# Performance work log

Hardware: AMD Instinct MI355X
Metric: run time of the kernel (lower is better)

The kernel has to match this reference:

```python
import jax, jax.numpy as jnp
import numpy as np

B, T, D, H, DK, DV, FF = 4, 1024, 1024, 16, 64, 64, 4096


def setup_inputs() -> dict:
    key = jax.random.key(0)
    ks = jax.random.split(key, 16)
    sc = 0.02  # init scale (original uses uninitialized torch.empty; use small randn)
    n = lambda k, shape: jax.random.normal(k, shape, jnp.float32) * sc
    return dict(
        x=jax.random.normal(ks[0], (B, T, D), jnp.float32),
        y=jax.random.normal(ks[1], (B, T, D), jnp.float32),
        Wq1=n(ks[2], (H, D, DK)), Wk1=n(ks[3], (H, D, DK)),
        Wv1=n(ks[4], (H, D, DV)), Wo1=n(ks[5], (D, D)),
        Wq2=n(ks[6], (H, D, DK)), Wk2=n(ks[7], (H, D, DK)),
        Wv2=n(ks[8], (H, D, DV)), Wo2=n(ks[9], (D, D)),
        W_in=n(ks[10], (FF, D)), b_in=jnp.zeros((FF,), jnp.float32),
        W_out=n(ks[11], (D, FF)), b_out=jnp.zeros((D,), jnp.float32),
    )


def _mha(q, k, v, Wq, Wk, Wv, Wo):
    # per-head projections: (B,T,D) x (H,D,dk) -> (B,H,T,dk)
    WQ = jnp.einsum('btd,hdk->bhtk', q, Wq)
    WK = jnp.einsum('bsd,hdk->bhsk', k, Wk)
    WV = jnp.einsum('bsd,hdv->bhsv', v, Wv)
    scores = jnp.einsum('bhtk,bhsk->bhts', WQ, WK) / jnp.sqrt(jnp.float32(DK))
    # NOTE: original code softmaxes over dim=2 (the QUERY axis), kept faithfully
    attn = jax.nn.softmax(scores, axis=2)
    partial = jnp.einsum('bhts,bhsv->bhtv', attn, WV)
    partial = partial.transpose(0, 2, 1, 3).reshape(q.shape[0], q.shape[1], -1)  # (B,T,H*dv)
    return partial @ Wo


def _sub_norm(o):
    mean = o.mean(-1, keepdims=True)
    std = o.std(-1, ddof=1, keepdims=True)  # torch.std default is unbiased
    return o - mean - std  # faithful: subtract (not divide by) std


def reference(x, y, Wq1, Wk1, Wv1, Wo1, Wq2, Wk2, Wv2, Wo2, W_in, b_in, W_out, b_out):
    out1 = _sub_norm(_mha(y, y, y, Wq1, Wk1, Wv1, Wo1) + y)
    out2 = _sub_norm(_mha(y, x, x, Wq2, Wk2, Wv2, Wo2) + out1)
    ff = jax.nn.relu(y @ W_in.T + b_in) @ W_out.T + b_out  # FFN applied to y, as in source
    return _sub_norm(ff + out2)
```

## Files before the change

kernel.cpp:

```cpp
#include <hip/hip_runtime.h>


typedef unsigned short u16;
typedef __bf16 bf16x8 __attribute__((ext_vector_type(8)));
typedef float f32x4 __attribute__((ext_vector_type(4)));

__device__ __forceinline__ u16 f2bf(float f) {
    unsigned int u = __float_as_uint(f);
    u += 0x7fffu + ((u >> 16) & 1u);
    return (u16)(u >> 16);
}
__device__ __forceinline__ float bf2f(u16 b) {
    return __uint_as_float(((unsigned int)b) << 16);
}

typedef __attribute__((address_space(1))) const void* as1cv;
typedef __attribute__((address_space(3))) void* as3v;
__device__ __forceinline__ void gl_lds16(const void* g, void* l) {
    __builtin_amdgcn_global_load_lds((as1cv)g, (as3v)l, 16, 0, 0);
}

__global__ __launch_bounds__(256) void mega_pack_k(
    const float* __restrict__ yf, u16* __restrict__ yb,
    const float* __restrict__ xf, u16* __restrict__ xb,
    const float* __restrict__ W_in, u16* __restrict__ Winb,
    const float* __restrict__ W_out, u16* __restrict__ Woutb,
    const float* __restrict__ Wq1, const float* __restrict__ Wk1,
    const float* __restrict__ Wv1, const float* __restrict__ Wq2,
    u16* __restrict__ W1cat,
    const float* __restrict__ Wk2, const float* __restrict__ Wv2,
    u16* __restrict__ Wkv2t,
    const float* __restrict__ Wo1, u16* __restrict__ Wo1t,
    const float* __restrict__ Wo2, u16* __restrict__ Wo2t)
{
    __shared__ float tile[64][65];
    int id = blockIdx.x;
    if (id < 16384) {
        int j = id >> 12, local = id & 4095;
        const float* in; u16* out;
        switch (j) {
            case 0:  in = yf;    out = yb;    break;
            case 1:  in = xf;    out = xb;    break;
            case 2:  in = W_in;  out = Winb;  break;
            default: in = W_out; out = Woutb; break;
        }
        long i = (long)local * 256 + threadIdx.x;
        float4 v = reinterpret_cast<const float4*>(in)[i];
        ushort4 o;
        o.x = f2bf(v.x); o.y = f2bf(v.y); o.z = f2bf(v.z); o.w = f2bf(v.w);
        reinterpret_cast<ushort4*>(out)[i] = o;
        return;
    }
    int t = id - 16384;
    int pj = t >> 8, local = t & 255;
    const float* in; u16* out;
    int Q, R, bx, by, bz;
    if (pj < 6) {
        switch (pj) {
            case 0:  in = Wq1; out = W1cat;           break;
            case 1:  in = Wk1; out = W1cat + 1048576; break;
            case 2:  in = Wv1; out = W1cat + 2097152; break;
            case 3:  in = Wq2; out = W1cat + 3145728; break;
            case 4:  in = Wk2; out = Wkv2t;           break;
            default: in = Wv2; out = Wkv2t + 1048576; break;
        }
        Q = 1024; R = 64; bx = 0; by = local & 15; bz = local >> 4;
    } else {
        in = (pj == 6) ? Wo1 : Wo2; out = (pj == 6) ? Wo1t : Wo2t;
        Q = 1024; R = 1024; bx = local & 15; by = local >> 4; bz = 0;
    }
    int r0 = bx * 64, q0 = by * 64;
    int tx = threadIdx.x & 63, ty = threadIdx.x >> 6;
    const float* inp = in + ((long)bz * Q + q0) * R + r0;
    #pragma unroll
    for (int i = 0; i < 64; i += 4)
        tile[ty + i][tx] = inp[(long)(ty + i) * R + tx];
    __syncthreads();
    u16* outp = out + ((long)bz * R + r0) * Q + q0;
    #pragma unroll
    for (int i = 0; i < 64; i += 4)
        outp[(long)(ty + i) * Q + tx] = f2bf(tile[tx][ty + i]);
}

__global__ __launch_bounds__(256) void transpose_scale_k(
    const u16* __restrict__ in, long ld_in, long z_in,
    u16* __restrict__ out, long ld_out, long z_out,
    const float* __restrict__ csum) {
    __shared__ u16 tile[64][66];
    int z = blockIdx.z;
    const u16* inz = in + (long)z * z_in;
    u16* outz = out + (long)z * z_out;
    int r0 = blockIdx.y * 64;
    int c0 = blockIdx.x * 64;
    int tx = threadIdx.x & 63, ty = threadIdx.x >> 6;
    #pragma unroll
    for (int i = 0; i < 64; i += 4)
        tile[ty + i][tx] = inz[(long)(r0 + ty + i) * ld_in + c0 + tx];
    __syncthreads();
    #pragma unroll
    for (int i = 0; i < 64; i += 4) {
        int orow = c0 + ty + i;
        float f = bf2f(tile[tx][ty + i]) / csum[(long)z * 16384 + (orow >> 6) * 1024 + r0 + tx];
        outz[(long)orow * ld_out + r0 + tx] = f2bf(f);
    }
}

template<int BM, int BN, int BK, int WM, int WN, int OUT_BF16, int EPI, int SWZ, int KS>
__global__ __launch_bounds__(256) void gemm_k(
    const u16* __restrict__ A, long lda, long a_zin, long a_zout,
    const u16* __restrict__ B, long ldb, long b_zin, long b_zout,
    void* __restrict__ Cv, long ldc, long c_zin, long c_zout,
    int zin, int K, float alpha, const float* __restrict__ bias,
    float* __restrict__ csum)
{
    static_assert(BK == 64, "staging assumes BK=64");
    constexpr int WTM = BM / WM;
    constexpr int WTN = BN / WN;
    constexpr int TM = WTM / 16;
    constexpr int TN = WTN / 16;
    __shared__ __align__(16) u16 smem[(BM + BN) * BK];
    u16* As = smem;
    u16* Bs = smem + BM * BK;

    int bx, by, z;
    if (SWZ == 4) {
        int L = blockIdx.x;
        if (KS > 1) { z = L >> 9; L &= 511; } else { z = 0; }
        by = (L & 7) * 4 + ((L >> 3) & 3);
        bx = L >> 5;
    } else {
        bx = blockIdx.x; by = blockIdx.y; z = blockIdx.z;
    }
    int zi = z % zin, zo = z / zin;
    A += (long)zi * a_zin + (long)zo * a_zout;
    B += (long)zi * b_zin + (long)zo * b_zout;
    long coff = (long)zi * c_zin + (long)zo * c_zout;

    int tid = threadIdx.x;
    int lane = tid & 63;
    int wave = tid >> 6;
    int wm = wave / WN, wn = wave % WN;
    long bm0 = (long)by * BM, bn0 = (long)bx * BN;

    f32x4 acc[TM][TN];
    #pragma unroll
    for (int i = 0; i < TM; ++i)
        #pragma unroll
        for (int j = 0; j < TN; ++j) {
            acc[i][j][0] = 0.f; acc[i][j][1] = 0.f;
            acc[i][j][2] = 0.f; acc[i][j][3] = 0.f;
        }

    int r16 = lane & 15;
    int quad = lane >> 4;
    int l8 = lane >> 3;
    int gsw = ((lane & 7) ^ l8) * 8;

    constexpr int ASTR = BM / 8;
    constexpr int BSTR = BN / 8;

    for (int k0 = 0; k0 < K; k0 += BK) {
        #pragma unroll
        for (int s = wave; s < ASTR; s += 4)
            gl_lds16(&A[(bm0 + s * 8 + l8) * lda + k0 + gsw], &As[s * 512]);
        #pragma unroll
        for (int s = wave; s < BSTR; s += 4)
            gl_lds16(&B[(bn0 + s * 8 + l8) * ldb + k0 + gsw], &Bs[s * 512]);
        __syncthreads();
        #pragma unroll
        for (int kk = 0; kk < BK; kk += 32) {
            int cb = (kk >> 3) + quad;
            bf16x8 av[TM], bv[TN];
            #pragma unroll
            for (int i = 0; i < TM; ++i) {
                int r = wm * WTM + i * 16 + r16;
                av[i] = *reinterpret_cast<const bf16x8*>(&As[r * 64 + ((cb ^ (r & 7)) * 8)]);
            }
            #pragma unroll
            for (int j = 0; j < TN; ++j) {
                int r = wn * WTN + j * 16 + r16;
                bv[j] = *reinterpret_cast<const bf16x8*>(&Bs[r * 64 + ((cb ^ (r & 7)) * 8)]);
            }
            #pragma unroll
            for (int i = 0; i < TM; ++i)
                #pragma unroll
                for (int j = 0; j < TN; ++j)
                    acc[i][j] = __builtin_amdgcn_mfma_f32_16x16x32_bf16(av[i], bv[j], acc[i][j], 0, 0, 0);
        }
        __syncthreads();
    }

    int rb = quad * 4;

    if (EPI == 4) {
        float csl[TN];
        #pragma unroll
        for (int j = 0; j < TN; ++j) csl[j] = 0.f;
        #pragma unroll
        for (int i = 0; i < TM; ++i)
            #pragma unroll
            for (int j = 0; j < TN; ++j)
                #pragma unroll
                for (int r = 0; r < 4; ++r)
                    csl[j] += __expf(acc[i][j][r] * alpha);
        #pragma unroll
        for (int j = 0; j < TN; ++j) {
            float cs = csl[j];
            cs += __shfl_xor(cs, 16, 64);
            cs += __shfl_xor(cs, 32, 64);
            if (quad == 0) {
                long col = bn0 + wn * WTN + j * 16 + r16;
                atomicAdd(&csum[((long)zo * zin + zi) * 1024 + col], cs);
            }
        }
        return;
    }

    constexpr int EB = OUT_BF16 ? 2 : 4;
    constexpr int CH = 16 / EB;
    constexpr int STRIDE = BN + CH;
    constexpr int LDSB = (BM + BN) * BK * 2;
    constexpr int EPASS = (BM * STRIDE * EB > LDSB) ? 2 : 1;
    constexpr int RPP = BM / EPASS;
    static_assert(RPP * STRIDE * EB <= LDSB, "epilogue tile overflows LDS");
    static_assert(EPASS == 1 || (WM == 2 && WTM == RPP), "pass/wave row alignment");
    constexpr int CPR = BN / CH;
    constexpr int NCH = RPP * CPR / 256;
    static_assert(RPP * CPR % 256 == 0, "store mapping");

    float* Ef = reinterpret_cast<float*>(smem);
    char* Cb = reinterpret_cast<char*>(Cv);

    for (int pass = 0; pass < EPASS; ++pass) {
        int p0 = pass * RPP;
        __syncthreads();
        #pragma unroll
        for (int i = 0; i < TM; ++i) {
            #pragma unroll
            for (int j = 0; j < TN; ++j) {
                int lcol = wn * WTN + j * 16 + r16;
                float bsv = (EPI == 1 || EPI == 2) ? bias[bn0 + lcol] : 0.f;
                #pragma unroll
                for (int r = 0; r < 4; ++r) {
                    int lrow = wm * WTM + i * 16 + rb + r;
                    if ((unsigned)(lrow - p0) < (unsigned)RPP) {
                        float v = acc[i][j][r] * alpha;
                        if (EPI == 1) { v += bsv; v = v > 0.f ? v : 0.f; }
                        else if (EPI == 2) { v += bsv; }
                        if (OUT_BF16) smem[(lrow - p0) * STRIDE + lcol] = f2bf(v);
                        else          Ef[(lrow - p0) * STRIDE + lcol] = v;
                    }
                }
            }
        }
        __syncthreads();
        #pragma unroll
        for (int c = 0; c < NCH; ++c) {
            int cid = tid + c * 256;
            int row = cid / CPR, ch = cid - row * CPR;
            int4 v = *reinterpret_cast<const int4*>(
                reinterpret_cast<const char*>(smem) + (row * STRIDE + ch * CH) * EB);
            long gidx = coff + (bm0 + p0 + row) * ldc + bn0 + ch * CH;
            *reinterpret_cast<int4*>(Cb + gidx * EB) = v;
        }
    }
}


__device__ __forceinline__ void bar_raw() {
    asm volatile("" ::: "memory");
    __builtin_amdgcn_s_barrier();
    asm volatile("" ::: "memory");
}

template<int N> __device__ __forceinline__ void vmw() {
    if constexpr (N == 10) asm volatile("s_waitcnt vmcnt(10)" ::: "memory");
    else if constexpr (N == 8) asm volatile("s_waitcnt vmcnt(8)" ::: "memory");
    else if constexpr (N == 4) asm volatile("s_waitcnt vmcnt(4)" ::: "memory");
    else if constexpr (N == 2) asm volatile("s_waitcnt vmcnt(2)" ::: "memory");
    else if constexpr (N == 0) asm volatile("s_waitcnt vmcnt(0)" ::: "memory");
}

__device__ __forceinline__ void stage_half(const u16* __restrict__ base, long ld, int kt,
                                           u16* __restrict__ lds, int half, int wave) {
    const u16* src = base + (long)kt * 64;
    #pragma unroll
    for (int u = 0; u < 2; ++u) {
        int s = half * 16 + u * 8 + wave;
        gl_lds16(src + (long)(s * 8) * ld, lds + s * 512);
    }
}

template<int IH>
__device__ __forceinline__ void read_a8(bf16x8 (&av)[4][2], const u16* __restrict__ As,
                                        int wm, int r16, int quad) {
    #pragma unroll
    for (int ii = 0; ii < 4; ++ii) {
        int r = IH * 128 + wm * 64 + ii * 16 + r16;
        #pragma unroll
        for (int kx = 0; kx < 2; ++kx)
            av[ii][kx] = *reinterpret_cast<const bf16x8*>(&As[r * 64 + (((kx * 4 + quad) ^ (r & 7)) * 8)]);
    }
}

template<int JH>
__device__ __forceinline__ void read_b8(bf16x8 (&bv)[2][2], const u16* __restrict__ Bs,
                                        int wn, int r16, int quad) {
    #pragma unroll
    for (int j = 0; j < 2; ++j) {
        int r = JH * 128 + wn * 32 + j * 16 + r16;
        #pragma unroll
        for (int kx = 0; kx < 2; ++kx)
            bv[j][kx] = *reinterpret_cast<const bf16x8*>(&Bs[r * 64 + (((kx * 4 + quad) ^ (r & 7)) * 8)]);
    }
}

template<int IH, int JH>
__device__ __forceinline__ void mfma_q(f32x4 (&acc)[2][4][2][2],
                                       const bf16x8 (&av)[4][2], const bf16x8 (&bv)[2][2]) {
    #pragma unroll
    for (int kx = 0; kx < 2; ++kx)
        #pragma unroll
        for (int ii = 0; ii < 4; ++ii)
            #pragma unroll
            for (int j = 0; j < 2; ++j)
                acc[IH][ii][JH][j] = __builtin_amdgcn_mfma_f32_16x16x32_bf16(
                    av[ii][kx], bv[j][kx], acc[IH][ii][JH][j], 0, 0, 0);
}

template<int MODE>
__device__ __forceinline__ void tile_iter(
    int t, f32x4 (&acc)[2][4][2][2], bf16x8 (&av)[4][2], bf16x8 (&bvh)[2][2][2],
    u16* __restrict__ smem, const u16* __restrict__ Ab, long lda,
    const u16* __restrict__ Bb, long ldb, int wave, int wm, int wn, int r16, int quad)
{
    u16* As0 = smem + (t & 1) * 32768;
    u16* Bs0 = As0 + 16384;
    u16* As1 = smem + ((t + 1) & 1) * 32768;
    read_a8<0>(av, As0, wm, r16, quad);
    read_b8<0>(bvh[0], Bs0, wn, r16, quad);
    if (MODE < 2) stage_half(Ab, lda, t + 1, As1, 1, wave);
    vmw<MODE == 0 ? 10 : (MODE == 1 ? 10 : 2)>();
    bar_raw(); __builtin_amdgcn_sched_barrier(0);
    __builtin_amdgcn_s_setprio(1);
    mfma_q<0, 0>(acc, av, bvh[0]);
    __builtin_amdgcn_s_setprio(0);
    __builtin_amdgcn_sched_barrier(0);
    bar_raw();
    read_b8<1>(bvh[1], Bs0, wn, r16, quad);
    if (MODE == 0) stage_half(Ab, lda, t + 2, As0, 0, wave);
    vmw<MODE == 0 ? 10 : (MODE == 1 ? 8 : 0)>();
    bar_raw(); __builtin_amdgcn_sched_barrier(0);
    __builtin_amdgcn_s_setprio(1);
    mfma_q<0, 1>(acc, av, bvh[1]);
    __builtin_amdgcn_s_setprio(0);
    __builtin_amdgcn_sched_barrier(0);
    bar_raw();
    read_a8<1>(av, As0, wm, r16, quad);
    if (MODE == 0) stage_half(Bb, ldb, t + 2, Bs0, 0, wave);
    bar_raw(); __builtin_amdgcn_sched_barrier(0);
    __builtin_amdgcn_s_setprio(1);
    mfma_q<1, 0>(acc, av, bvh[0]);
    __builtin_amdgcn_s_setprio(0);
    __builtin_amdgcn_sched_barrier(0);
    bar_raw();
    if (MODE == 0) stage_half(Bb, ldb, t + 2, Bs0, 1, wave);
    if (MODE < 2) vmw<MODE == 0 ? 10 : 4>();
    bar_raw(); __builtin_amdgcn_sched_barrier(0);
    __builtin_amdgcn_s_setprio(1);
    mfma_q<1, 1>(acc, av, bvh[1]);
    __builtin_amdgcn_s_setprio(0);
    __builtin_amdgcn_sched_barrier(0);
    bar_raw();
}

template<int NT, int KS, int EPI, int OUT_BF16, int SPLITN>
__global__ __launch_bounds__(512, 2) void gemm8_k(
    const u16* __restrict__ A, long lda,
    const u16* __restrict__ B, long ldb,
    void* __restrict__ Cv, void* __restrict__ Cv2, long ldc,
    int K, float alpha, const float* __restrict__ bias, long czs)
{
    __shared__ __align__(16) u16 smem[65536];

    int L = blockIdx.x;
    int z = 0;
    if (KS > 1) { z = L / (16 * NT); L -= z * 16 * NT; }
    int by = (L & 7) * 2 + ((L >> 3) & 1);
    int bx = L >> 4;
    if (KS > 1) { A += (long)z * K; B += (long)z * K; }

    int tid = threadIdx.x;
    int lane = tid & 63, wave = tid >> 6;
    int wm = wave >> 2, wn = wave & 3;
    int r16 = lane & 15, quad = lane >> 4, l8 = lane >> 3;
    int gsw = ((lane & 7) ^ l8) * 8;
    long bm0 = (long)by * 256, bn0 = (long)bx * 256;
    const u16* Ab = A + (bm0 + l8) * lda + gsw;
    const u16* Bb = B + (bn0 + l8) * ldb + gsw;

    f32x4 acc[2][4][2][2];
    #pragma unroll
    for (int a0 = 0; a0 < 2; ++a0)
        #pragma unroll
        for (int a1 = 0; a1 < 4; ++a1)
            #pragma unroll
            for (int a2 = 0; a2 < 2; ++a2)
                #pragma unroll
                for (int a3 = 0; a3 < 2; ++a3) {
                    acc[a0][a1][a2][a3][0] = 0.f; acc[a0][a1][a2][a3][1] = 0.f;
                    acc[a0][a1][a2][a3][2] = 0.f; acc[a0][a1][a2][a3][3] = 0.f;
                }
    bf16x8 av[4][2];
    bf16x8 bvh[2][2][2];

    int T = K >> 6;

    stage_half(Ab, lda, 0, smem,         0, wave);
    stage_half(Bb, ldb, 0, smem + 16384, 0, wave);
    stage_half(Bb, ldb, 0, smem + 16384, 1, wave);
    stage_half(Ab, lda, 0, smem,         1, wave);
    stage_half(Ab, lda, 1, smem + 32768, 0, wave);
    stage_half(Bb, ldb, 1, smem + 49152, 0, wave);
    stage_half(Bb, ldb, 1, smem + 49152, 1, wave);
    vmw<10>();
    bar_raw();

    for (int t = 0; t < T - 2; ++t)
        tile_iter<0>(t, acc, av, bvh, smem, Ab, lda, Bb, ldb, wave, wm, wn, r16, quad);
    tile_iter<1>(T - 2, acc, av, bvh, smem, Ab, lda, Bb, ldb, wave, wm, wn, r16, quad);
    tile_iter<2>(T - 1, acc, av, bvh, smem, Ab, lda, Bb, ldb, wave, wm, wn, r16, quad);

    constexpr int EB = OUT_BF16 ? 2 : 4;
    constexpr int EPASS = OUT_BF16 ? 1 : 2;
    bool sec = SPLITN && (bx >= NT / 2);
    char* Cb;
    long bnc = bn0;
    if (SPLITN) {
        Cb = reinterpret_cast<char*>(sec ? Cv2 : Cv);
        if (sec) bnc = bn0 - (long)(NT / 2) * 256;
    } else {
        Cb = reinterpret_cast<char*>((KS > 1 && z >= 2) ? Cv2 : Cv);
        if (KS > 1) Cb += (long)(z & 1) * czs * EB;
    }
    bool do_bias = (EPI == 1) || sec;
    float bsv[2][2];
    if (do_bias) {
        #pragma unroll
        for (int jh = 0; jh < 2; ++jh)
            #pragma unroll
            for (int j = 0; j < 2; ++j)
                bsv[jh][j] = bias[bnc + jh * 128 + wn * 32 + j * 16 + r16];
    }
    u16* sm16 = smem;
    float* smf = reinterpret_cast<float*>(smem);
    #pragma unroll
    for (int pass = 0; pass < EPASS; ++pass) {
        bar_raw();
        #pragma unroll
        for (int ih = 0; ih < 2; ++ih) {
            if (EPASS == 2 && ih != pass) continue;
            #pragma unroll
            for (int ii = 0; ii < 4; ++ii)
                #pragma unroll
                for (int jh = 0; jh < 2; ++jh)
                    #pragma unroll
                    for (int j = 0; j < 2; ++j)
                        #pragma unroll
                        for (int r = 0; r < 4; ++r) {
                            int lrow = (EPASS == 2 ? 0 : ih * 128) + wm * 64 + ii * 16 + quad * 4 + r;
                            int lcol = jh * 128 + wn * 32 + j * 16 + r16;
                            float v = acc[ih][ii][jh][j][r] * alpha;
                            if (do_bias) { v += bsv[jh][j]; v = v > 0.f ? v : 0.f; }
                            int scol = lcol ^ ((lrow & 7) * 8);
                            if (OUT_BF16) sm16[lrow * 256 + scol] = f2bf(v);
                            else          smf[lrow * 256 + scol] = v;
                        }
        }
        bar_raw();
        constexpr int CH = 16 / EB;
        constexpr int CPR = 256 / CH;
        constexpr int NCH = (OUT_BF16 ? 256 : 128) * CPR / 512;
        #pragma unroll
        for (int c = 0; c < NCH; ++c) {
            int cid = tid + c * 512;
            int row = cid / CPR, ch = cid - row * CPR;
            int col = (ch * CH) ^ ((row & 7) * 8);
            int4 v = *reinterpret_cast<const int4*>(
                reinterpret_cast<const char*>(smem) + ((long)row * 256 + col) * EB);
            long grow = bm0 + pass * 128 + row;
            *reinterpret_cast<int4*>(Cb + (grow * ldc + bnc + ch * CH) * EB) = v;
        }
    }
}

__global__ __launch_bounds__(256) void attn_pv_k(
    const u16* __restrict__ Qg, long ldq, long qbz,
    const u16* __restrict__ Kg, long ldk, long kbz,
    const u16* __restrict__ Vg,
    u16* __restrict__ outg)
{
    __shared__ __align__(16) u16 Qs[128 * 64];
    __shared__ __align__(16) u16 Ks[2][64 * 64];
    __shared__ __align__(16) u16 Vs[2][64 * 64];
    __shared__ __align__(16) u16 Es[128 * 64];

    int L = blockIdx.x;
    int h  = (L & 7) * 2 + ((L >> 3) & 1);
    int tb = (L >> 4) & 7;
    int b  = L >> 7;

    const u16* Q  = Qg + (long)b * qbz + h * 64;
    const u16* Kp = Kg + (long)b * kbz + h * 64;
    const u16* Vp = Vg + (long)b * 1048576 + (long)h * 65536;
    u16* outp = outg + (long)b * 1048576 + (long)tb * 131072 + h * 64;

    int tid = threadIdx.x, lane = tid & 63, wave = tid >> 6;
    int wm = wave >> 1, wn = wave & 1;
    int r16 = lane & 15, quad = lane >> 4, l8 = lane >> 3;
    int gsw = ((lane & 7) ^ l8) * 8;
    long t0 = (long)tb * 128;

    #pragma unroll
    for (int s = wave; s < 16; s += 4)
        gl_lds16(&Q[(t0 + s * 8 + l8) * ldq + gsw], &Qs[s * 512]);
    #pragma unroll
    for (int s = wave; s < 8; s += 4) {
        gl_lds16(&Kp[(long)(s * 8 + l8) * ldk + gsw], &Ks[0][s * 512]);
        gl_lds16(&Vp[(long)(s * 8 + l8) * 1024 + gsw], &Vs[0][s * 512]);
    }

    f32x4 acc[4][2];
    #pragma unroll
    for (int i = 0; i < 4; ++i)
        #pragma unroll
        for (int j = 0; j < 2; ++j) {
            acc[i][j][0] = 0.f; acc[i][j][1] = 0.f;
            acc[i][j][2] = 0.f; acc[i][j][3] = 0.f;
        }

    for (int sc = 0; sc < 16; ++sc) {
        const u16* Ksc = Ks[sc & 1];
        const u16* Vsc = Vs[sc & 1];
        if (sc < 15) {
            int nc = sc + 1;
            u16* Kn = Ks[nc & 1];
            u16* Vn = Vs[nc & 1];
            #pragma unroll
            for (int s = wave; s < 8; s += 4) {
                gl_lds16(&Kp[(long)(nc * 64 + s * 8 + l8) * ldk + gsw], &Kn[s * 512]);
                gl_lds16(&Vp[(long)(s * 8 + l8) * 1024 + nc * 64 + gsw], &Vn[s * 512]);
            }
            asm volatile("s_waitcnt vmcnt(4)" ::: "memory");
        } else {
            asm volatile("s_waitcnt vmcnt(0)" ::: "memory");
        }
        bar_raw();

        f32x4 e[4][2];
        #pragma unroll
        for (int i = 0; i < 4; ++i)
            #pragma unroll
            for (int j = 0; j < 2; ++j) {
                e[i][j][0] = 0.f; e[i][j][1] = 0.f;
                e[i][j][2] = 0.f; e[i][j][3] = 0.f;
            }
        #pragma unroll
        for (int kk = 0; kk < 64; kk += 32) {
            int cb = (kk >> 3) + quad;
            bf16x8 av[4], bv[2];
            #pragma unroll
            for (int i = 0; i < 4; ++i) {
                int r = wm * 64 + i * 16 + r16;
                av[i] = *reinterpret_cast<const bf16x8*>(&Qs[r * 64 + ((cb ^ (r & 7)) * 8)]);
            }
            #pragma unroll
            for (int j = 0; j < 2; ++j) {
                int r = wn * 32 + j * 16 + r16;
                bv[j] = *reinterpret_cast<const bf16x8*>(&Ksc[r * 64 + ((cb ^ (r & 7)) * 8)]);
            }
            #pragma unroll
            for (int i = 0; i < 4; ++i)
                #pragma unroll
                for (int j = 0; j < 2; ++j)
                    e[i][j] = __builtin_amdgcn_mfma_f32_16x16x32_bf16(av[i], bv[j], e[i][j], 0, 0, 0);
        }
        #pragma unroll
        for (int i = 0; i < 4; ++i)
            #pragma unroll
            for (int j = 0; j < 2; ++j) {
                int lcol = wn * 32 + j * 16 + r16;
                #pragma unroll
                for (int r = 0; r < 4; ++r) {
                    int lrow = wm * 64 + i * 16 + quad * 4 + r;
                    float v = __expf(e[i][j][r] * 0.125f);
                    Es[lrow * 64 + (((lcol >> 3) ^ (lrow & 7)) * 8) + (lcol & 7)] = f2bf(v);
                }
            }
        asm volatile("s_waitcnt lgkmcnt(0)" ::: "memory");
        bar_raw();

        #pragma unroll
        for (int kk = 0; kk < 64; kk += 32) {
            int cb = (kk >> 3) + quad;
            bf16x8 av[4], bv[2];
            #pragma unroll
            for (int i = 0; i < 4; ++i) {
                int r = wm * 64 + i * 16 + r16;
                av[i] = *reinterpret_cast<const bf16x8*>(&Es[r * 64 + ((cb ^ (r & 7)) * 8)]);
            }
            #pragma unroll
            for (int j = 0; j < 2; ++j) {
                int r = wn * 32 + j * 16 + r16;
                bv[j] = *reinterpret_cast<const bf16x8*>(&Vsc[r * 64 + ((cb ^ (r & 7)) * 8)]);
            }
            #pragma unroll
            for (int i = 0; i < 4; ++i)
                #pragma unroll
                for (int j = 0; j < 2; ++j)
                    acc[i][j] = __builtin_amdgcn_mfma_f32_16x16x32_bf16(av[i], bv[j], acc[i][j], 0, 0, 0);
        }
        bar_raw();
    }

    #pragma unroll
    for (int i = 0; i < 4; ++i)
        #pragma unroll
        for (int j = 0; j < 2; ++j) {
            int lcol = wn * 32 + j * 16 + r16;
            #pragma unroll
            for (int r = 0; r < 4; ++r) {
                int lrow = wm * 64 + i * 16 + quad * 4 + r;
                outp[(long)lrow * 1024 + lcol] = f2bf(acc[i][j][r]);
            }
        }
}

template<int NP, int BIAS>
__global__ __launch_bounds__(256) void addsn_k(const float* __restrict__ parts,
                                               const float* __restrict__ parts2,
                                               long pstride,
                                               const float* __restrict__ resid,
                                               const float* __restrict__ bias,
                                               float* __restrict__ out) {
    __shared__ float sm[8];
    long row = blockIdx.x;
    int tid = threadIdx.x;
    float4 x = reinterpret_cast<const float4*>(resid + row * 1024)[tid];
    #pragma unroll
    for (int p = 0; p < NP; ++p) {
        const float* src = (p < 2) ? (parts + p * pstride) : (parts2 + (p - 2) * pstride);
        float4 a = reinterpret_cast<const float4*>(src + row * 1024)[tid];
        x.x += a.x; x.y += a.y; x.z += a.z; x.w += a.w;
    }
    if (BIAS) {
        float4 bb = reinterpret_cast<const float4*>(bias)[tid];
        x.x += bb.x; x.y += bb.y; x.z += bb.z; x.w += bb.w;
    }
    float s = x.x + x.y + x.z + x.w;
    for (int o = 32; o > 0; o >>= 1) s += __shfl_down(s, o, 64);
    int lane = tid & 63, w = tid >> 6;
    if (lane == 0) sm[w] = s;
    __syncthreads();
    float mean = (sm[0] + sm[1] + sm[2] + sm[3]) * (1.f / 1024.f);
    float d0 = x.x - mean, d1 = x.y - mean, d2 = x.z - mean, d3 = x.w - mean;
    float q = d0 * d0 + d1 * d1 + d2 * d2 + d3 * d3;
    for (int o = 32; o > 0; o >>= 1) q += __shfl_down(q, o, 64);
    if (lane == 0) sm[w + 4] = q;
    __syncthreads();
    float sd = sqrtf((sm[4] + sm[5] + sm[6] + sm[7]) * (1.f / 1023.f));
    float4 ov;
    ov.x = d0 - sd; ov.y = d1 - sd; ov.z = d2 - sd; ov.w = d3 - sd;
    reinterpret_cast<float4*>(out + row * 1024)[tid] = ov;
}


extern "C" void kernel_launch(void* const* d_in, const int* in_sizes, int n_in,
                              void* d_out, int out_size, void* d_ws, size_t ws_size,
                              hipStream_t stream) {
    (void)in_sizes; (void)n_in; (void)out_size; (void)ws_size;
    const float* xf   = (const float*)d_in[0];
    const float* yf   = (const float*)d_in[1];
    const float* Wq1  = (const float*)d_in[2];
    const float* Wk1  = (const float*)d_in[3];
    const float* Wv1  = (const float*)d_in[4];
    const float* Wo1  = (const float*)d_in[5];
    const float* Wq2  = (const float*)d_in[6];
    const float* Wk2  = (const float*)d_in[7];
    const float* Wv2  = (const float*)d_in[8];
    const float* Wo2  = (const float*)d_in[9];
    const float* W_in = (const float*)d_in[10];
    const float* b_in = (const float*)d_in[11];
    const float* W_out= (const float*)d_in[12];
    const float* b_out= (const float*)d_in[13];

    char* p = (char*)d_ws;
    auto alloc = [&](size_t bytes) { char* r = p; p += bytes; return r; };
    u16*   yb    = (u16*)alloc(8388608);
    u16*   xb    = (u16*)alloc(8388608);
    u16*   W1cat = (u16*)alloc(8388608);
    u16*   Winb  = (u16*)alloc(8388608);
    u16*   Wkv2t = (u16*)alloc(4194304);
    u16*   Wo1t  = (u16*)alloc(2097152);
    u16*   Wo2t  = (u16*)alloc(2097152);
    u16*   Woutb = (u16*)alloc(8388608);
    u16*   QKV   = (u16*)alloc(33554432);
    u16*   KV2   = (u16*)alloc(16777216);
    u16*   Vt    = (u16*)alloc(8388608);
    u16*   Pb    = (u16*)alloc(33554432);
    float* csum  = (float*)alloc(262144);
    u16*   part  = (u16*)alloc(8388608);
    float* gout  = (float*)alloc(33554432);
    float* out1  = (float*)alloc(16777216);

    mega_pack_k<<<18432, 256, 0, stream>>>(
        yf, yb, xf, xb, W_in, Winb, W_out, Woutb,
        Wq1, Wk1, Wv1, Wq2, W1cat, Wk2, Wv2, Wkv2t,
        Wo1, Wo1t, Wo2, Wo2t);

    auto run_attention = [&](const u16* Q, long ldq, long qbz,
                             const u16* Kp, long ldk, long kbz,
                             const u16* Vp, long ldv, long vbz) {
        hipMemsetAsync(csum, 0, 262144, stream);
        gemm_k<128,128,64,2,2,1,4,0,1><<<dim3(8, 8, 64), 256, 0, stream>>>(
            Q, ldq, 64L, qbz, Kp, ldk, 64L, kbz,
            (void*)Pb, 1024L, 0L, 0L, 16, 64, 0.125f, nullptr, csum);
        transpose_scale_k<<<dim3(16, 16, 4), 256, 0, stream>>>(
            Vp, ldv, vbz, Vt, 1024L, 1048576L, csum);
        attn_pv_k<<<512, 256, 0, stream>>>(Q, ldq, qbz, Kp, ldk, kbz, Vt, part);
    };

    gemm8_k<32,1,0,1,1><<<512, 512, 0, stream>>>(
        yb, 1024L, W1cat, 1024L, (void*)QKV, (void*)Pb, 4096L, 1024, 1.0f, b_in, 0L);
    gemm8_k<8,1,0,1,0><<<128, 512, 0, stream>>>(
        xb, 1024L, Wkv2t, 1024L, (void*)KV2, nullptr, 2048L, 1024, 1.0f, nullptr, 0L);

    run_attention(QKV, 4096L, 4194304L, QKV + 1024, 4096L, 4194304L, QKV + 2048, 4096L, 4194304L);
    gemm_k<128,64,64,2,2,0,0,4,2><<<dim3(2 * 512), 256, 0, stream>>>(
        part, 1024L, 0L, 512L, Wo1t, 1024L, 0L, 512L,
        (void*)gout, 1024L, 0L, 4194304L, 1, 512, 1.0f, nullptr, nullptr);
    addsn_k<2,0><<<4096, 256, 0, stream>>>(gout, nullptr, 4194304L, yf, nullptr, out1);

    run_attention(QKV + 3072, 4096L, 4194304L, KV2, 2048L, 2097152L, KV2 + 1024, 2048L, 2097152L);
    gemm_k<128,64,64,2,2,0,0,4,2><<<dim3(2 * 512), 256, 0, stream>>>(
        part, 1024L, 0L, 512L, Wo2t, 1024L, 0L, 512L,
        (void*)gout, 1024L, 0L, 4194304L, 1, 512, 1.0f, nullptr, nullptr);
    addsn_k<2,0><<<4096, 256, 0, stream>>>(gout, nullptr, 4194304L, out1, nullptr, (float*)d_out);

    gemm8_k<4,4,0,0,0><<<256, 512, 0, stream>>>(
        Pb, 4096L, Woutb, 4096L, (void*)gout, (void*)QKV, 1024L, 1024, 1.0f, nullptr, 4194304L);
    addsn_k<4,1><<<4096, 256, 0, stream>>>(gout, (const float*)QKV, 4194304L,
                                           (const float*)d_out, b_out, (float*)d_out);
}
```

Before: 508.0 us.

## Batch both attention blocks into merged launches and fold memset into pack kernel

Runs the two attention passes (self and cross) together: one QK gemm launch over 128 z-slices, one merged V transpose/scale, and one PV kernel over 1024 blocks. The two output-projection gemms now run as a single split-style gemm, and the csum zeroing moves into extra blocks of the pack kernel instead of a memset. Workspace buffers are aliased to fit the doubled intermediates. This cuts launch count and fills the GPU better with larger grids, at the cost of more memory and careful buffer reuse.

```diff
diff --git a/kernel.cpp b/kernel.cpp
--- a/kernel.cpp
+++ b/kernel.cpp
@@ -31,10 +31,17 @@
     const float* __restrict__ Wk2, const float* __restrict__ Wv2,
     u16* __restrict__ Wkv2t,
     const float* __restrict__ Wo1, u16* __restrict__ Wo1t,
-    const float* __restrict__ Wo2, u16* __restrict__ Wo2t)
+    const float* __restrict__ Wo2, u16* __restrict__ Wo2t,
+    float* __restrict__ csumz)
 {
     __shared__ float tile[64][65];
     int id = blockIdx.x;
+    if (id >= 18432) {
+        long i = (long)(id - 18432) * 256 + threadIdx.x;
+        float4 zz; zz.x = 0.f; zz.y = 0.f; zz.z = 0.f; zz.w = 0.f;
+        reinterpret_cast<float4*>(csumz)[i] = zz;
+        return;
+    }
     if (id < 16384) {
         int j = id >> 12, local = id & 4095;
         const float* in; u16* out;
@@ -82,36 +89,43 @@
         outp[(long)(ty + i) * Q + tx] = f2bf(tile[tx][ty + i]);
 }
 
-__global__ __launch_bounds__(256) void transpose_scale_k(
-    const u16* __restrict__ in, long ld_in, long z_in,
-    u16* __restrict__ out, long ld_out, long z_out,
-    const float* __restrict__ csum) {
+__global__ __launch_bounds__(256) void tscale2_k(
+    const u16* __restrict__ in1, long ld1, long zs1,
+    const u16* __restrict__ in2, long ld2, long zs2,
+    u16* __restrict__ Vt, const float* __restrict__ csum) {
     __shared__ u16 tile[64][66];
     int z = blockIdx.z;
-    const u16* inz = in + (long)z * z_in;
-    u16* outz = out + (long)z * z_out;
+    int m = z >> 2, zb = z & 3;
+    const u16* in; long ld, zs;
+    if (m) { in = in2; ld = ld2; zs = zs2; } else { in = in1; ld = ld1; zs = zs1; }
+    const u16* inz = in + (long)zb * zs;
+    u16* outz = Vt + (long)m * 4194304 + (long)zb * 1048576;
+    const float* cs = csum + m * 65536 + (long)zb * 16384;
     int r0 = blockIdx.y * 64;
     int c0 = blockIdx.x * 64;
     int tx = threadIdx.x & 63, ty = threadIdx.x >> 6;
     #pragma unroll
     for (int i = 0; i < 64; i += 4)
-        tile[ty + i][tx] = inz[(long)(r0 + ty + i) * ld_in + c0 + tx];
+        tile[ty + i][tx] = inz[(long)(r0 + ty + i) * ld + c0 + tx];
     __syncthreads();
     #pragma unroll
     for (int i = 0; i < 64; i += 4) {
         int orow = c0 + ty + i;
-        float f = bf2f(tile[tx][ty + i]) / csum[(long)z * 16384 + (orow >> 6) * 1024 + r0 + tx];
-        outz[(long)orow * ld_out + r0 + tx] = f2bf(f);
-    }
-}
-
-template<int BM, int BN, int BK, int WM, int WN, int OUT_BF16, int EPI, int SWZ, int KS>
+        float f = bf2f(tile[tx][ty + i]) / cs[(orow >> 6) * 1024 + r0 + tx];
+        outz[(long)orow * 1024 + r0 + tx] = f2bf(f);
+    }
+}
+
+template<int BM, int BN, int BK, int WM, int WN, int OUT_BF16, int EPI, int SWZ, int KS, int MRG>
 __global__ __launch_bounds__(256) void gemm_k(
     const u16* __restrict__ A, long lda, long a_zin, long a_zout,
     const u16* __restrict__ B, long ldb, long b_zin, long b_zout,
     void* __restrict__ Cv, long ldc, long c_zin, long c_zout,
     int zin, int K, float alpha, const float* __restrict__ bias,
-    float* __restrict__ csum)
+    float* __restrict__ csum,
+    const u16* __restrict__ A2, long lda2,
+    const u16* __restrict__ B2, long ldb2, long b_zout2,
+    float* __restrict__ csum2)
 {
     static_assert(BK == 64, "staging assumes BK=64");
     constexpr int WTM = BM / WM;
@@ -130,6 +144,10 @@
         bx = L >> 5;
     } else {
         bx = blockIdx.x; by = blockIdx.y; z = blockIdx.z;
+    }
+    if (MRG) {
+        int m2 = z >> 6; z &= 63;
+        if (m2) { A = A2; lda = lda2; B = B2; ldb = ldb2; b_zout = b_zout2; csum = csum2; }
     }
     int zi = z % zin, zo = z / zin;
     A += (long)zi * a_zin + (long)zo * a_zout;
@@ -494,11 +512,14 @@
     }
 }
 
+template<int MRG>
 __global__ __launch_bounds__(256) void attn_pv_k(
     const u16* __restrict__ Qg, long ldq, long qbz,
     const u16* __restrict__ Kg, long ldk, long kbz,
-    const u16* __restrict__ Vg,
-    u16* __restrict__ outg)
+    const u16* __restrict__ Vg, u16* __restrict__ outg,
+    const u16* __restrict__ Qg2,
+    const u16* __restrict__ Kg2, long ldk2, long kbz2,
+    const u16* __restrict__ Vg2, u16* __restrict__ outg2)
 {
     __shared__ __align__(16) u16 Qs[128 * 64];
     __shared__ __align__(16) u16 Ks[2][64 * 64];
@@ -506,6 +527,10 @@
     __shared__ __align__(16) u16 Es[128 * 64];
 
     int L = blockIdx.x;
+    if (MRG) {
+        int m = L >> 9; L &= 511;
+        if (m) { Qg = Qg2; Kg = Kg2; ldk = ldk2; kbz = kbz2; Vg = Vg2; outg = outg2; }
+    }
     int h  = (L & 7) * 2 + ((L >> 3) & 1);
     int tb = (L >> 4) & 7;
     int b  = L >> 7;
@@ -706,49 +731,51 @@
     u16*   Woutb = (u16*)alloc(8388608);
     u16*   QKV   = (u16*)alloc(33554432);
     u16*   KV2   = (u16*)alloc(16777216);
-    u16*   Vt    = (u16*)alloc(8388608);
     u16*   Pb    = (u16*)alloc(33554432);
-    float* csum  = (float*)alloc(262144);
-    u16*   part  = (u16*)alloc(8388608);
+    u16*   part  = (u16*)alloc(16777216);
     float* gout  = (float*)alloc(33554432);
-    float* out1  = (float*)alloc(16777216);
-
-    mega_pack_k<<<18432, 256, 0, stream>>>(
+    u16*   Vt    = yb;
+    float* csum  = gout;
+    float* out1  = (float*)part;
+    float* ffnC2 = (float*)yb;
+
+    mega_pack_k<<<18560, 256, 0, stream>>>(
         yf, yb, xf, xb, W_in, Winb, W_out, Woutb,
         Wq1, Wk1, Wv1, Wq2, W1cat, Wk2, Wv2, Wkv2t,
-        Wo1, Wo1t, Wo2, Wo2t);
-
-    auto run_attention = [&](const u16* Q, long ldq, long qbz,
-                             const u16* Kp, long ldk, long kbz,
-                             const u16* Vp, long ldv, long vbz) {
-        hipMemsetAsync(csum, 0, 262144, stream);
-        gemm_k<128,128,64,2,2,1,4,0,1><<<dim3(8, 8, 64), 256, 0, stream>>>(
-            Q, ldq, 64L, qbz, Kp, ldk, 64L, kbz,
-            (void*)Pb, 1024L, 0L, 0L, 16, 64, 0.125f, nullptr, csum);
-        transpose_scale_k<<<dim3(16, 16, 4), 256, 0, stream>>>(
-            Vp, ldv, vbz, Vt, 1024L, 1048576L, csum);
-        attn_pv_k<<<512, 256, 0, stream>>>(Q, ldq, qbz, Kp, ldk, kbz, Vt, part);
-    };
+        Wo1, Wo1t, Wo2, Wo2t, csum);
 
     gemm8_k<32,1,0,1,1><<<512, 512, 0, stream>>>(
         yb, 1024L, W1cat, 1024L, (void*)QKV, (void*)Pb, 4096L, 1024, 1.0f, b_in, 0L);
     gemm8_k<8,1,0,1,0><<<128, 512, 0, stream>>>(
         xb, 1024L, Wkv2t, 1024L, (void*)KV2, nullptr, 2048L, 1024, 1.0f, nullptr, 0L);
 
-    run_attention(QKV, 4096L, 4194304L, QKV + 1024, 4096L, 4194304L, QKV + 2048, 4096L, 4194304L);
-    gemm_k<128,64,64,2,2,0,0,4,2><<<dim3(2 * 512), 256, 0, stream>>>(
-        part, 1024L, 0L, 512L, Wo1t, 1024L, 0L, 512L,
-        (void*)gout, 1024L, 0L, 4194304L, 1, 512, 1.0f, nullptr, nullptr);
-    addsn_k<2,0><<<4096, 256, 0, stream>>>(gout, nullptr, 4194304L, yf, nullptr, out1);
-
-    run_attention(QKV + 3072, 4096L, 4194304L, KV2, 2048L, 2097152L, KV2 + 1024, 2048L, 2097152L);
-    gemm_k<128,64,64,2,2,0,0,4,2><<<dim3(2 * 512), 256, 0, stream>>>(
-        part, 1024L, 0L, 512L, Wo2t, 1024L, 0L, 512L,
-        (void*)gout, 1024L, 0L, 4194304L, 1, 512, 1.0f, nullptr, nullptr);
-    addsn_k<2,0><<<4096, 256, 0, stream>>>(gout, nullptr, 4194304L, out1, nullptr, (float*)d_out);
+    gemm_k<128,128,64,2,2,1,4,0,1,1><<<dim3(8, 8, 128), 256, 0, stream>>>(
+        QKV, 4096L, 64L, 4194304L,
+        QKV + 1024, 4096L, 64L, 4194304L,
+        (void*)Pb, 1024L, 0L, 0L, 16, 64, 0.125f, nullptr, csum,
+        QKV + 3072, 4096L,
+        KV2, 2048L, 2097152L,
+        csum + 65536);
+
+    tscale2_k<<<dim3(16, 16, 8), 256, 0, stream>>>(
+        QKV + 2048, 4096L, 4194304L,
+        KV2 + 1024, 2048L, 2097152L,
+        Vt, csum);
+
+    attn_pv_k<1><<<1024, 256, 0, stream>>>(
+        QKV, 4096L, 4194304L, QKV + 1024, 4096L, 4194304L, Vt, part,
+        QKV + 3072, KV2, 2048L, 2097152L, Vt + 4194304, part + 4194304);
+
+    gemm_k<128,64,64,2,2,0,0,4,2,0><<<1024, 256, 0, stream>>>(
+        part, 1024L, 0L, 4194304L, Wo1t, 1024L, 0L, 1048576L,
+        (void*)gout, 1024L, 0L, 4194304L, 1, 1024, 1.0f, nullptr, nullptr,
+        nullptr, 0L, nullptr, 0L, 0L, nullptr);
 
     gemm8_k<4,4,0,0,0><<<256, 512, 0, stream>>>(
-        Pb, 4096L, Woutb, 4096L, (void*)gout, (void*)QKV, 1024L, 1024, 1.0f, nullptr, 4194304L);
-    addsn_k<4,1><<<4096, 256, 0, stream>>>(gout, (const float*)QKV, 4194304L,
+        Pb, 4096L, Woutb, 4096L, (void*)QKV, (void*)ffnC2, 1024L, 1024, 1.0f, nullptr, 4194304L);
+
+    addsn_k<1,0><<<4096, 256, 0, stream>>>(gout, nullptr, 0L, yf, nullptr, out1);
+    addsn_k<1,0><<<4096, 256, 0, stream>>>(gout + 4194304, nullptr, 0L, out1, nullptr, (float*)d_out);
+    addsn_k<4,1><<<4096, 256, 0, stream>>>((const float*)QKV, ffnC2, 4194304L,
                                            (const float*)d_out, b_out, (float*)d_out);
 }
```

After: 481.7 us. 1.05x faster.
